# Performance work log

Hardware: AMD Instinct MI355X
Metric: run time of the kernel (lower is better)

## Reference

```python
import jax, jax.numpy as jnp
import numpy as np
from jax import lax

K = 16  # knn_k


def _mlp(x, W1, b1, W2, b2):
    h = jax.nn.gelu(x @ W1 + b1, approximate=False)  # torch nn.GELU default = exact
    return h @ W2 + b2


def setup_inputs() -> dict:
    key = jax.random.key(0)
    ks = jax.random.split(key, 10)
    B, N, F, H = 8, 4096, 64, 128

    def xav(k, shape):
        fan_in = shape[0]
        return (jax.random.normal(k, shape, jnp.float32) / np.sqrt(fan_in)).astype(jnp.float32)

    return {
        "coords": jax.random.normal(ks[0], (B, N, 3), jnp.float32),
        "features": jax.random.normal(ks[1], (B, N, F), jnp.float32),
        "inv_W1": xav(ks[2], (6, H)), "inv_b1": jnp.zeros((H,), jnp.float32),
        "inv_W2": xav(ks[3], (H, H)), "inv_b2": jnp.zeros((H,), jnp.float32),
        "feat_W1": xav(ks[4], (F, H)), "feat_b1": jnp.zeros((H,), jnp.float32),
        "feat_W2": xav(ks[5], (H, H)), "feat_b2": jnp.zeros((H,), jnp.float32),
        "sh_W1": xav(ks[6], (2 * H, H)), "sh_b1": jnp.zeros((H,), jnp.float32),
        "sh_W2": xav(ks[7], (H, H)), "sh_b2": jnp.zeros((H,), jnp.float32),
        "g0_W": xav(ks[8], (H, 1)), "g0_b": jnp.zeros((1,), jnp.float32),
    }


def _local_geometry(coords):
    # coords: [B,N,3]
    B, N, _ = coords.shape
    k = min(K, N - 1)
    # squared pairwise distances (monotone in euclidean dist -> same kNN indices)
    sq = jnp.sum(coords * coords, axis=-1)                    # [B,N]
    dist2 = sq[:, :, None] + sq[:, None, :] - 2.0 * jnp.einsum("bnd,bmd->bnm", coords, coords)
    dist2 = lax.stop_gradient(dist2)
    eye = jnp.eye(N, dtype=bool)
    dist2 = jnp.where(eye[None], jnp.inf, dist2)
    _, idx = lax.top_k(-dist2, k)                             # smallest-k -> [B,N,k]
    neighbors = jax.vmap(lambda c, i: c[i])(coords, idx)      # [B,N,k,3]
    relative = neighbors - coords[:, :, None, :]              # [B,N,k,3]
    cov = jnp.einsum("bnki,bnkj->bnij", relative, relative) / float(k)  # [B,N,3,3]
    evals, evecs = jnp.linalg.eigh(cov)                       # ascending
    normals = evecs[..., 0]                                   # smallest-eigval eigenvector, [B,N,3]
    center = coords.mean(axis=1, keepdims=True)
    outward = coords - center
    orient = jnp.sign(jnp.sum(normals * outward, axis=-1, keepdims=True))
    orient = jnp.where(orient == 0, 1.0, orient)
    normals = normals * orient
    normals = normals / jnp.maximum(jnp.linalg.norm(normals, axis=-1, keepdims=True), 1e-6)
    radius = jnp.linalg.norm(relative, axis=-1).mean(axis=-1, keepdims=True)   # [B,N,1]
    centered_radius = jnp.linalg.norm(outward, axis=-1, keepdims=True)
    eig_sum = jnp.maximum(evals.sum(axis=-1, keepdims=True), 1e-6)
    dominance = evals[..., 2:3] / eig_sum
    invariants = jnp.concatenate([evals, radius, centered_radius, dominance], axis=-1)  # [B,N,6]
    return normals, invariants


def reference(coords, features, inv_W1, inv_b1, inv_W2, inv_b2,
              feat_W1, feat_b1, feat_W2, feat_b2,
              sh_W1, sh_b1, sh_W2, sh_b2, g0_W, g0_b):
    normals, invariants = _local_geometry(coords)
    inv_h = _mlp(invariants, inv_W1, inv_b1, inv_W2, inv_b2)
    feat_h = _mlp(features, feat_W1, feat_b1, feat_W2, feat_b2)
    hidden = _mlp(jnp.concatenate([inv_h, feat_h], axis=-1), sh_W1, sh_b1, sh_W2, sh_b2)
    scalar = hidden @ g0_W + g0_b                                   # grade 0, [B,N,1]
    plane = jnp.stack([normals[..., 0], normals[..., 1], -normals[..., 2],
                       -jnp.sum(coords * normals, axis=-1)], axis=-1)  # grade 1, [B,N,4]
    biv = jnp.concatenate([normals, jnp.zeros_like(normals)], axis=-1)  # grade 2, [B,N,6]
    point = jnp.concatenate([coords, jnp.ones(coords.shape[:-1] + (1,), coords.dtype)], axis=-1)  # grade 3 OPNS point
    zero4 = jnp.zeros(coords.shape[:-1] + (1,), coords.dtype)            # grade 4
    return jnp.concatenate([scalar, plane, biv, point, zero4], axis=-1)  # [B,N,16]
```

## Files before the change

### kernel.cpp

```cpp
#include <hip/hip_runtime.h>
#include <hip/hip_bf16.h>

#define BB 8
#define NN 4096
#define FF 64
#define HH 128
#define KNN 16

typedef __attribute__((ext_vector_type(8))) short bf16x8;
typedef __attribute__((ext_vector_type(4))) short bf16x4;
typedef __attribute__((ext_vector_type(4))) float f32x4;

#define OFF_iW2 0
#define OFF_fW1 16384
#define OFF_fW2 24576
#define OFF_sW1 40960
#define OFF_sW2 73728
#define HI_SZ   90112

__device__ __forceinline__ float sq3(float x, float y, float z) {
    return fmaf(z, z, fmaf(y, y, __fmul_rn(x, x)));
}
__device__ __forceinline__ float dist2f(float px, float py, float pz, float psq, float4 cc) {
    float t = fmaf(pz, cc.z, fmaf(py, cc.y, __fmul_rn(px, cc.x)));
    return __fsub_rn(__fadd_rn(psq, cc.w), __fmul_rn(2.0f, t));
}

__device__ __forceinline__ short f2bf(float x) {
    unsigned u = __float_as_uint(x);
    u += 0x7fffu + ((u >> 16) & 1u);
    return (short)(u >> 16);
}
__device__ __forceinline__ float bf2f(short s) {
    return __uint_as_float(((unsigned)(unsigned short)s) << 16);
}

extern "C" __global__ __launch_bounds__(256)
void k_prep(const float* __restrict__ coords, float4* __restrict__ coords4, float* __restrict__ center,
            const float* __restrict__ iW2, const float* __restrict__ fW1,
            const float* __restrict__ fW2, const float* __restrict__ sW1,
            const float* __restrict__ sW2, short* __restrict__ wbf) {
    const int bx = blockIdx.x, tid = threadIdx.x;
    __shared__ float rx[256], ry[256], rz[256];
    if (bx < 8) {
        const int b = bx;
        float sx = 0.f, sy = 0.f, sz = 0.f;
        for (int n = tid; n < NN; n += 256) {
            const float* c = coords + (size_t)(b * NN + n) * 3;
            float x = c[0], y = c[1], z = c[2];
            coords4[b * NN + n] = make_float4(x, y, z, sq3(x, y, z));
            sx += x; sy += y; sz += z;
        }
        rx[tid] = sx; ry[tid] = sy; rz[tid] = sz;
        __syncthreads();
        for (int s = 128; s > 0; s >>= 1) {
            if (tid < s) { rx[tid] += rx[tid + s]; ry[tid] += ry[tid + s]; rz[tid] += rz[tid + s]; }
            __syncthreads();
        }
        if (tid == 0) {
            center[b * 4 + 0] = rx[0] * (1.0f / NN);
            center[b * 4 + 1] = ry[0] * (1.0f / NN);
            center[b * 4 + 2] = rz[0] * (1.0f / NN);
        }
    } else {
        const int wb = bx - 8;
        const int w = wb >> 4;
        const int xb = wb & 15;
        const float* W; int K; int off;
        if (w == 0)      { W = iW2; K = 128; off = OFF_iW2; }
        else if (w == 1) { W = fW1; K = 64;  off = OFF_fW1; }
        else if (w == 2) { W = fW2; K = 128; off = OFF_fW2; }
        else if (w == 3) { W = sW1; K = 256; off = OFF_sW1; }
        else             { W = sW2; K = 128; off = OFF_sW2; }
        short* hi = wbf + off;
        short* lo = wbf + HI_SZ + off;
        const int total = K * 128;
        for (int e = xb * 256 + tid; e < total; e += 4096) {
            int j = e & 7, lane = (e >> 3) & 63, ct = (e >> 9) & 7, kb = e >> 12;
            int k = kb * 32 + (lane >> 4) * 8 + j;
            int n = ct * 16 + (lane & 15);
            float v = W[k * 128 + n];
            short h = f2bf(v);
            float r = v - bf2f(h);
            hi[e] = h; lo[e] = f2bf(r);
        }
    }
}

#define JROT(app, aqq, apq, arp, arq, vp0, vp1, vp2, vq0, vq1, vq2) { \
    float tau_ = (aqq - app) / (2.0f * apq); \
    float tt_ = copysignf(1.0f, tau_) / (fabsf(tau_) + sqrtf(1.0f + tau_ * tau_)); \
    if (apq == 0.0f) tt_ = 0.0f; \
    float cc_ = 1.0f / sqrtf(1.0f + tt_ * tt_); \
    float ss_ = tt_ * cc_; \
    float app_n = cc_*cc_*app - 2.0f*cc_*ss_*apq + ss_*ss_*aqq; \
    float aqq_n = ss_*ss_*app + 2.0f*cc_*ss_*apq + cc_*cc_*aqq; \
    float apq_n = cc_*ss_*(app - aqq) + (cc_*cc_ - ss_*ss_)*apq; \
    float arp_n = cc_*arp - ss_*arq; \
    float arq_n = ss_*arp + cc_*arq; \
    app = app_n; aqq = aqq_n; apq = apq_n; arp = arp_n; arq = arq_n; \
    float t0_ = cc_*vp0 - ss_*vq0, t1_ = cc_*vp1 - ss_*vq1, t2_ = cc_*vp2 - ss_*vq2; \
    vq0 = ss_*vp0 + cc_*vq0; vq1 = ss_*vp1 + cc_*vq1; vq2 = ss_*vp2 + cc_*vq2; \
    vp0 = t0_; vp1 = t1_; vp2 = t2_; }

#define SWAPF(a, b) { float sw_ = a; a = b; b = sw_; }

__device__ __forceinline__ void ce(float& a, float& b) {
    float mn = fminf(a, b);
    b = fmaxf(a, b);
    a = mn;
}

__device__ __forceinline__ void sort16(float (&d)[16]) {
    ce(d[0],d[1]); ce(d[2],d[3]); ce(d[0],d[2]); ce(d[1],d[3]); ce(d[1],d[2]);
    ce(d[4],d[5]); ce(d[6],d[7]); ce(d[4],d[6]); ce(d[5],d[7]); ce(d[5],d[6]);
    ce(d[0],d[4]); ce(d[2],d[6]); ce(d[2],d[4]);
    ce(d[1],d[5]); ce(d[3],d[7]); ce(d[3],d[5]);
    ce(d[1],d[2]); ce(d[3],d[4]); ce(d[5],d[6]);
    ce(d[8],d[9]); ce(d[10],d[11]); ce(d[8],d[10]); ce(d[9],d[11]); ce(d[9],d[10]);
    ce(d[12],d[13]); ce(d[14],d[15]); ce(d[12],d[14]); ce(d[13],d[15]); ce(d[13],d[14]);
    ce(d[8],d[12]); ce(d[10],d[14]); ce(d[10],d[12]);
    ce(d[9],d[13]); ce(d[11],d[15]); ce(d[11],d[13]);
    ce(d[9],d[10]); ce(d[11],d[12]); ce(d[13],d[14]);
    ce(d[0],d[8]); ce(d[4],d[12]); ce(d[4],d[8]);
    ce(d[2],d[10]); ce(d[6],d[14]); ce(d[6],d[10]);
    ce(d[2],d[4]); ce(d[6],d[8]); ce(d[10],d[12]);
    ce(d[1],d[9]); ce(d[5],d[13]); ce(d[5],d[9]);
    ce(d[3],d[11]); ce(d[7],d[15]); ce(d[7],d[11]);
    ce(d[3],d[5]); ce(d[7],d[9]); ce(d[11],d[13]);
    ce(d[1],d[2]); ce(d[3],d[4]); ce(d[5],d[6]); ce(d[7],d[8]);
    ce(d[9],d[10]); ce(d[11],d[12]); ce(d[13],d[14]);
}

__device__ __forceinline__ void merge16(float (&dk)[16], float (&d)[16]) {
#pragma unroll
    for (int i = 0; i < 8; i++) {
        float a  = fminf(dk[i], d[15 - i]);
        float b2 = fminf(dk[15 - i], d[i]);
        d[i] = a; d[15 - i] = b2;
    }
#pragma unroll
    for (int j = 8; j > 0; j >>= 1)
#pragma unroll
        for (int i = 0; i < 16; i++) {
            int l = i ^ j;
            if (l > i) ce(d[i], d[l]);
        }
#pragma unroll
    for (int i = 0; i < 16; i++) dk[i] = d[i];
}

__device__ __forceinline__ void sort16i(int (&d)[16]) {
#pragma unroll
    for (int k = 2; k <= 16; k <<= 1) {
#pragma unroll
        for (int j = k >> 1; j > 0; j >>= 1) {
#pragma unroll
            for (int i = 0; i < 16; i++) {
                int l = i ^ j;
                if (l > i) {
                    int a = d[i], bq = d[l];
                    int mn = a < bq ? a : bq;
                    int mx = a < bq ? bq : a;
                    if ((i & k) == 0) { d[i] = mn; d[l] = mx; }
                    else              { d[i] = mx; d[l] = mn; }
                }
            }
        }
    }
}

__device__ __forceinline__ float gelu_exact(float x) {
    return 0.5f * x * (1.0f + erff(x * 0.70710678118654752440f));
}

template <int KB, bool INIT>
__device__ __forceinline__ void gemm_mfma(const short* Ab, const short* __restrict__ whi,
                                          const short* __restrict__ wlo,
                                          const float* __restrict__ bias,
                                          int wid, int lane, f32x4 acc[2]) {
    const int m16 = lane & 15, quad = lane >> 4;
    if (INIT) {
        float b0 = bias[wid * 16 + m16];
        acc[0] = (f32x4){b0, b0, b0, b0};
        acc[1] = acc[0];
    }
#pragma unroll 1
    for (int kb = 0; kb < KB; kb++) {
        bf16x8 a0 = *(const bf16x8*)(Ab + m16 * 136 + kb * 32 + quad * 8);
        bf16x8 a1 = *(const bf16x8*)(Ab + (m16 + 16) * 136 + kb * 32 + quad * 8);
        const int off = ((kb * 8 + wid) * 64 + lane) * 8;
        bf16x8 bh = *(const bf16x8*)(whi + off);
        bf16x8 bl = *(const bf16x8*)(wlo + off);
        acc[0] = __builtin_amdgcn_mfma_f32_16x16x32_bf16(a0, bh, acc[0], 0, 0, 0);
        acc[0] = __builtin_amdgcn_mfma_f32_16x16x32_bf16(a0, bl, acc[0], 0, 0, 0);
        acc[1] = __builtin_amdgcn_mfma_f32_16x16x32_bf16(a1, bh, acc[1], 0, 0, 0);
        acc[1] = __builtin_amdgcn_mfma_f32_16x16x32_bf16(a1, bl, acc[1], 0, 0, 0);
    }
}

__device__ __forceinline__ void acc_to_bf(short* dst, f32x4 acc[2], int wid, int lane, bool dogelu) {
    const int m16 = lane & 15, quad = lane >> 4;
#pragma unroll
    for (int mt = 0; mt < 2; mt++)
#pragma unroll
        for (int i = 0; i < 4; i++) {
            float v = acc[mt][i];
            if (dogelu) v = gelu_exact(v);
            dst[(mt * 16 + quad * 4 + i) * 136 + wid * 16 + m16] = f2bf(v);
        }
}

extern "C" __global__ __launch_bounds__(512, 8)
void k_fused(const float4* __restrict__ coords4, const float* __restrict__ center,
             const float* __restrict__ features, const short* __restrict__ wbf,
             const float* __restrict__ iW1, const float* __restrict__ ib1,
             const float* __restrict__ ib2,
             const float* __restrict__ fb1, const float* __restrict__ fb2,
             const float* __restrict__ sb1, const float* __restrict__ sb2,
             const float* __restrict__ gW, const float* __restrict__ gb,
             float* __restrict__ out) {
    const int blk = blockIdx.x;
    const int b = blk >> 7;
    const int chunk = blk & 127;
    const int tid = threadIdx.x;
    const int h = tid & 15;
    const int pid = tid >> 4;
    const int n = chunk * 32 + pid;
    const float4* __restrict__ C = coords4 + b * NN;

    __shared__ __align__(16) char smem[20352];
    unsigned short* slist = (unsigned short*)(smem);
    unsigned short* tlist = (unsigned short*)(smem + 1024);
    int* cnt_s = (int*)(smem + 1536);
    int* cnt_t = (int*)(smem + 1664);
    float* inv8 = (float*)(smem + 1792);
    float* sc   = (float*)(smem + 2816);
    short* Abf  = (short*)(smem + 2944);
    short* FHbf = (short*)(smem + 11648);

    if (tid < 32) { cnt_s[tid] = 0; cnt_t[tid] = 0; }

    float4 me = C[n];
    const float px = me.x, py = me.y, pz = me.z, psq = me.w;
    const float INF = __builtin_inff();
    const int self_j = ((n & 15) == h) ? (n >> 4) : 256;

    float dk[KNN];
#pragma unroll
    for (int i = 0; i < KNN; i++) dk[i] = INF;

    for (int bt = 0; bt < 16; bt++) {
        float d[16];
#pragma unroll
        for (int i = 0; i < 16; i++) {
            float4 cc = C[(bt * 16 + i) * 16 + h];
            float dd = dist2f(px, py, pz, psq, cc);
            d[i] = (bt * 16 + i) == self_j ? INF : dd;
        }
        sort16(d);
        merge16(dk, d);
    }

#pragma unroll
    for (int m = 1; m <= 8; m <<= 1) {
        float o[16];
#pragma unroll
        for (int i = 0; i < KNN; i++) o[i] = __shfl_xor(dk[i], m);
        merge16(dk, o);
    }
    const float d15 = dk[15];

    __syncthreads();

#pragma unroll 4
    for (int j = 0; j < 256; j++) {
        float4 cc = C[j * 16 + h];
        float d = dist2f(px, py, pz, psq, cc);
        if (j != self_j && d <= d15) {
            if (d < d15) {
                int pos = atomicAdd(&cnt_s[pid], 1);
                if (pos < 16) slist[pid * 16 + pos] = (unsigned short)(j * 16 + h);
            } else {
                int pos = atomicAdd(&cnt_t[pid], 1);
                if (pos < 8) tlist[pid * 8 + pos] = (unsigned short)(j * 16 + h);
            }
        }
    }
    __syncthreads();

    if (tid < 32) {
        const int np = chunk * 32 + tid;
        float4 pme = C[np];
        int ns = cnt_s[tid]; ns = ns > 15 ? 15 : ns;
        int ids[16];
#pragma unroll
        for (int j = 0; j < 16; j++) {
            int tj = j - ns; tj = tj < 0 ? 0 : (tj > 7 ? 7 : tj);
            int sid = (int)slist[tid * 16 + j];
            int tie = (int)tlist[tid * 8 + tj];
            ids[j] = (j < ns) ? sid : tie;
        }
        sort16i(ids);

        float cxx = 0.f, cxy = 0.f, cxz = 0.f, cyy = 0.f, cyz = 0.f, czz = 0.f, radsum = 0.f;
#pragma unroll
        for (int j = 0; j < KNN; j++) {
            float4 cc = C[ids[j]];
            float rx = __fsub_rn(cc.x, pme.x), ry = __fsub_rn(cc.y, pme.y), rz = __fsub_rn(cc.z, pme.z);
            cxx = __fadd_rn(cxx, __fmul_rn(rx, rx));
            cxy = __fadd_rn(cxy, __fmul_rn(rx, ry));
            cxz = __fadd_rn(cxz, __fmul_rn(rx, rz));
            cyy = __fadd_rn(cyy, __fmul_rn(ry, ry));
            cyz = __fadd_rn(cyz, __fmul_rn(ry, rz));
            czz = __fadd_rn(czz, __fmul_rn(rz, rz));
            float rr = __fadd_rn(__fadd_rn(__fmul_rn(rx, rx), __fmul_rn(ry, ry)), __fmul_rn(rz, rz));
            radsum = __fadd_rn(radsum, sqrtf(rr));
        }
        const float inv_k = 1.0f / KNN;
        float a00 = cxx * inv_k, a01 = cxy * inv_k, a02 = cxz * inv_k;
        float a11 = cyy * inv_k, a12 = cyz * inv_k, a22 = czz * inv_k;

        float V00 = 1.f, V01 = 0.f, V02 = 0.f;
        float V10 = 0.f, V11 = 1.f, V12 = 0.f;
        float V20 = 0.f, V21 = 0.f, V22 = 1.f;
        for (int sweep = 0; sweep < 6; sweep++) {
            JROT(a00, a11, a01, a02, a12, V00, V10, V20, V01, V11, V21);
            JROT(a00, a22, a02, a01, a12, V00, V10, V20, V02, V12, V22);
            JROT(a11, a22, a12, a01, a02, V01, V11, V21, V02, V12, V22);
        }
        float e0 = a00, e1 = a11, e2 = a22;
        float x0 = V00, y0 = V10, z0 = V20;
        float x1 = V01, y1 = V11, z1 = V21;
        float x2 = V02, y2 = V12, z2 = V22;
        if (e0 > e1) { SWAPF(e0, e1); SWAPF(x0, x1); SWAPF(y0, y1); SWAPF(z0, z1); }
        if (e1 > e2) { SWAPF(e1, e2); SWAPF(x1, x2); SWAPF(y1, y2); SWAPF(z1, z2); }
        if (e0 > e1) { SWAPF(e0, e1); SWAPF(x0, x1); SWAPF(y0, y1); SWAPF(z0, z1); }

        float cx = center[b * 4 + 0], cy = center[b * 4 + 1], cz = center[b * 4 + 2];
        float ox = __fsub_rn(pme.x, cx), oy = __fsub_rn(pme.y, cy), oz = __fsub_rn(pme.z, cz);
        float dt = __fadd_rn(__fadd_rn(__fmul_rn(x0, ox), __fmul_rn(y0, oy)), __fmul_rn(z0, oz));
        float sgn = (dt >= 0.0f) ? 1.0f : -1.0f;
        x0 *= sgn; y0 *= sgn; z0 *= sgn;
        float nrm = sqrtf(__fadd_rn(__fadd_rn(__fmul_rn(x0, x0), __fmul_rn(y0, y0)), __fmul_rn(z0, z0)));
        float den = fmaxf(nrm, 1e-6f);
        x0 = x0 / den; y0 = y0 / den; z0 = z0 / den;

        float radius = radsum * inv_k;
        float crad = sqrtf(__fadd_rn(__fadd_rn(__fmul_rn(ox, ox), __fmul_rn(oy, oy)), __fmul_rn(oz, oz)));
        float esum = fmaxf(__fadd_rn(__fadd_rn(e0, e1), e2), 1e-6f);
        float dom = e2 / esum;

        float* ip = inv8 + tid * 8;
        ip[0] = e0; ip[1] = e1; ip[2] = e2; ip[3] = radius; ip[4] = crad; ip[5] = dom;
        ip[6] = 0.f; ip[7] = 0.f;

        float pd = __fadd_rn(__fadd_rn(__fmul_rn(pme.x, x0), __fmul_rn(pme.y, y0)), __fmul_rn(pme.z, z0));
        float4* o = (float4*)(out + (size_t)(b * NN + np) * 16);
        o[0] = make_float4(0.0f, x0, y0, -z0);
        o[1] = make_float4(-pd, x0, y0, z0);
        o[2] = make_float4(0.0f, 0.0f, 0.0f, pme.x);
        o[3] = make_float4(pme.y, pme.z, 1.0f, 0.0f);
        sc[tid] = gb[0];
    }
    __syncthreads();

    const int wid = tid >> 6, lane = tid & 63;
    const short* w_iW2h = wbf + OFF_iW2; const short* w_iW2l = wbf + HI_SZ + OFF_iW2;
    const short* w_fW1h = wbf + OFF_fW1; const short* w_fW1l = wbf + HI_SZ + OFF_fW1;
    const short* w_fW2h = wbf + OFF_fW2; const short* w_fW2l = wbf + HI_SZ + OFF_fW2;
    const short* w_sW1h = wbf + OFF_sW1; const short* w_sW1l = wbf + HI_SZ + OFF_sW1;
    const short* w_sW2h = wbf + OFF_sW2; const short* w_sW2l = wbf + HI_SZ + OFF_sW2;
    f32x4 acc[2];

    {
        int row = tid >> 4, c4 = (tid & 15) * 4;
        const float* s = features + (size_t)(b * NN + chunk * 32 + row) * FF + c4;
        float4 v = *(const float4*)s;
        bf16x4 pk;
        pk[0] = f2bf(v.x); pk[1] = f2bf(v.y); pk[2] = f2bf(v.z); pk[3] = f2bf(v.w);
        *(bf16x4*)(Abf + row * 136 + c4) = pk;
    }
    __syncthreads();

    gemm_mfma<2, true>(Abf, w_fW1h, w_fW1l, fb1, wid, lane, acc);
    __syncthreads();
    acc_to_bf(Abf, acc, wid, lane, true);
    __syncthreads();

    gemm_mfma<4, true>(Abf, w_fW2h, w_fW2l, fb2, wid, lane, acc);
    __syncthreads();
    acc_to_bf(FHbf, acc, wid, lane, false);

    {
        const int cg = tid & 31, pg = tid >> 5;
        const int c0 = cg * 4, p0 = pg * 2;
        float4 bb = *(const float4*)(ib1 + c0);
        float a2[2][4];
#pragma unroll
        for (int i = 0; i < 2; i++) { a2[i][0] = bb.x; a2[i][1] = bb.y; a2[i][2] = bb.z; a2[i][3] = bb.w; }
#pragma unroll
        for (int k = 0; k < 6; k++) {
            float4 w = *(const float4*)(iW1 + k * HH + c0);
#pragma unroll
            for (int i = 0; i < 2; i++) {
                float a = inv8[(p0 + i) * 8 + k];
                a2[i][0] = fmaf(a, w.x, a2[i][0]);
                a2[i][1] = fmaf(a, w.y, a2[i][1]);
                a2[i][2] = fmaf(a, w.z, a2[i][2]);
                a2[i][3] = fmaf(a, w.w, a2[i][3]);
            }
        }
#pragma unroll
        for (int i = 0; i < 2; i++) {
            bf16x4 pk;
            pk[0] = f2bf(gelu_exact(a2[i][0])); pk[1] = f2bf(gelu_exact(a2[i][1]));
            pk[2] = f2bf(gelu_exact(a2[i][2])); pk[3] = f2bf(gelu_exact(a2[i][3]));
            *(bf16x4*)(Abf + (p0 + i) * 136 + c0) = pk;
        }
    }
    __syncthreads();

    gemm_mfma<4, true>(Abf, w_iW2h, w_iW2l, ib2, wid, lane, acc);
    __syncthreads();
    acc_to_bf(Abf, acc, wid, lane, false);
    __syncthreads();

    gemm_mfma<4, true>(Abf, w_sW1h, w_sW1l, sb1, wid, lane, acc);
    gemm_mfma<4, false>(FHbf, w_sW1h + 16384, w_sW1l + 16384, nullptr, wid, lane, acc);
    __syncthreads();
    acc_to_bf(Abf, acc, wid, lane, true);
    __syncthreads();

    gemm_mfma<4, true>(Abf, w_sW2h, w_sW2l, sb2, wid, lane, acc);
    {
        const int m16 = lane & 15, quad = lane >> 4;
        float g = gW[wid * 16 + m16];
#pragma unroll
        for (int mt = 0; mt < 2; mt++)
#pragma unroll
            for (int i = 0; i < 4; i++)
                atomicAdd(&sc[mt * 16 + quad * 4 + i], acc[mt][i] * g);
    }
    __syncthreads();
    if (tid < 32) out[(size_t)(b * NN + chunk * 32 + tid) * 16] = sc[tid];
}

extern "C" void kernel_launch(void* const* d_in, const int* in_sizes, int n_in,
                              void* d_out, int out_size, void* d_ws, size_t ws_size,
                              hipStream_t stream) {
    const float* coords   = (const float*)d_in[0];
    const float* features = (const float*)d_in[1];
    const float* iW1 = (const float*)d_in[2],  * ib1 = (const float*)d_in[3];
    const float* iW2 = (const float*)d_in[4],  * ib2 = (const float*)d_in[5];
    const float* fW1 = (const float*)d_in[6],  * fb1 = (const float*)d_in[7];
    const float* fW2 = (const float*)d_in[8],  * fb2 = (const float*)d_in[9];
    const float* sW1 = (const float*)d_in[10], * sb1 = (const float*)d_in[11];
    const float* sW2 = (const float*)d_in[12], * sb2 = (const float*)d_in[13];
    const float* gW  = (const float*)d_in[14], * gb  = (const float*)d_in[15];
    float* out = (float*)d_out;

    float* ws = (float*)d_ws;
    float4* coords4 = (float4*)ws;
    float* center = ws + BB * NN * 4;
    short* wbf = (short*)((char*)d_ws + 524416);

    hipLaunchKernelGGL(k_prep, dim3(88), dim3(256), 0, stream,
                       coords, coords4, center, iW2, fW1, fW2, sW1, sW2, wbf);
    hipLaunchKernelGGL(k_fused, dim3(1024), dim3(512), 0, stream, coords4, center, features, wbf,
                       iW1, ib1, ib2, fb1, fb2, sb1, sb2, gW, gb, out);
}
```

Measured before the change: 295.9 us.

## Split fused kernel into kNN and MLP kernels, stage coords in LDS tiles

The fused kernel is split into a kNN/geometry kernel and an MLP kernel. The invariants are passed between them through a global workspace buffer. The kNN kernel now stages 1024-point coordinate tiles in shared memory and reads the candidates from LDS instead of from global memory in both the distance pass and the collection pass. Each kernel also gets its own smaller shared-memory footprint. The cost is an extra kernel launch, an extra global round trip for the invariants, and extra block barriers per tile.

```diff
diff --git a/kernel.cpp b/kernel.cpp
--- a/kernel.cpp
+++ b/kernel.cpp
@@ -170,6 +170,161 @@
     }
 }
 
+extern "C" __global__ __launch_bounds__(512, 8)
+void k_knn(const float4* __restrict__ coords4, const float* __restrict__ center,
+           float* __restrict__ inv8g, float* __restrict__ out) {
+    const int blk = blockIdx.x;
+    const int b = blk >> 7;
+    const int chunk = blk & 127;
+    const int tid = threadIdx.x;
+    const int h = tid & 15;
+    const int pid = tid >> 4;
+    const int n = chunk * 32 + pid;
+    const float4* __restrict__ C = coords4 + b * NN;
+
+    __shared__ __align__(16) float4 tile[1024];
+    __shared__ unsigned short slist[512];
+    __shared__ unsigned short tlist[256];
+    __shared__ int cnt_s[32];
+    __shared__ int cnt_t[32];
+
+    if (tid < 32) { cnt_s[tid] = 0; cnt_t[tid] = 0; }
+
+    float4 me = C[n];
+    const float px = me.x, py = me.y, pz = me.z, psq = me.w;
+    const float INF = __builtin_inff();
+
+    float dk[KNN];
+#pragma unroll
+    for (int i = 0; i < KNN; i++) dk[i] = INF;
+
+    for (int r = 0; r < 4; r++) {
+        __syncthreads();
+        tile[tid] = C[r * 1024 + tid];
+        tile[tid + 512] = C[r * 1024 + tid + 512];
+        __syncthreads();
+#pragma unroll
+        for (int bt = 0; bt < 4; bt++) {
+            float d[16];
+#pragma unroll
+            for (int i = 0; i < 16; i++) {
+                float4 cc = tile[bt * 256 + i * 16 + h];
+                float dd = dist2f(px, py, pz, psq, cc);
+                int g = r * 1024 + bt * 256 + i * 16 + h;
+                d[i] = (g == n) ? INF : dd;
+            }
+            sort16(d);
+            merge16(dk, d);
+        }
+    }
+
+#pragma unroll
+    for (int m = 1; m <= 8; m <<= 1) {
+        float o[16];
+#pragma unroll
+        for (int i = 0; i < KNN; i++) o[i] = __shfl_xor(dk[i], m);
+        merge16(dk, o);
+    }
+    const float d15 = dk[15];
+
+    for (int r = 0; r < 4; r++) {
+        __syncthreads();
+        tile[tid] = C[r * 1024 + tid];
+        tile[tid + 512] = C[r * 1024 + tid + 512];
+        __syncthreads();
+#pragma unroll 4
+        for (int j16 = 0; j16 < 64; j16++) {
+            float4 cc = tile[j16 * 16 + h];
+            float d = dist2f(px, py, pz, psq, cc);
+            int g = r * 1024 + j16 * 16 + h;
+            if (g != n && d <= d15) {
+                if (d < d15) {
+                    int pos = atomicAdd(&cnt_s[pid], 1);
+                    if (pos < 16) slist[pid * 16 + pos] = (unsigned short)g;
+                } else {
+                    int pos = atomicAdd(&cnt_t[pid], 1);
+                    if (pos < 8) tlist[pid * 8 + pos] = (unsigned short)g;
+                }
+            }
+        }
+    }
+    __syncthreads();
+
+    if (tid < 32) {
+        const int np = chunk * 32 + tid;
+        float4 pme = C[np];
+        int ns = cnt_s[tid]; ns = ns > 15 ? 15 : ns;
+        int ids[16];
+#pragma unroll
+        for (int j = 0; j < 16; j++) {
+            int tj = j - ns; tj = tj < 0 ? 0 : (tj > 7 ? 7 : tj);
+            int sid = (int)slist[tid * 16 + j];
+            int tie = (int)tlist[tid * 8 + tj];
+            ids[j] = (j < ns) ? sid : tie;
+        }
+        sort16i(ids);
+
+        float cxx = 0.f, cxy = 0.f, cxz = 0.f, cyy = 0.f, cyz = 0.f, czz = 0.f, radsum = 0.f;
+#pragma unroll
+        for (int j = 0; j < KNN; j++) {
+            float4 cc = C[ids[j]];
+            float rx = __fsub_rn(cc.x, pme.x), ry = __fsub_rn(cc.y, pme.y), rz = __fsub_rn(cc.z, pme.z);
+            cxx = __fadd_rn(cxx, __fmul_rn(rx, rx));
+            cxy = __fadd_rn(cxy, __fmul_rn(rx, ry));
+            cxz = __fadd_rn(cxz, __fmul_rn(rx, rz));
+            cyy = __fadd_rn(cyy, __fmul_rn(ry, ry));
+            cyz = __fadd_rn(cyz, __fmul_rn(ry, rz));
+            czz = __fadd_rn(czz, __fmul_rn(rz, rz));
+            float rr = __fadd_rn(__fadd_rn(__fmul_rn(rx, rx), __fmul_rn(ry, ry)), __fmul_rn(rz, rz));
+            radsum = __fadd_rn(radsum, sqrtf(rr));
+        }
+        const float inv_k = 1.0f / KNN;
+        float a00 = cxx * inv_k, a01 = cxy * inv_k, a02 = cxz * inv_k;
+        float a11 = cyy * inv_k, a12 = cyz * inv_k, a22 = czz * inv_k;
+
+        float V00 = 1.f, V01 = 0.f, V02 = 0.f;
+        float V10 = 0.f, V11 = 1.f, V12 = 0.f;
+        float V20 = 0.f, V21 = 0.f, V22 = 1.f;
+        for (int sweep = 0; sweep < 6; sweep++) {
+            JROT(a00, a11, a01, a02, a12, V00, V10, V20, V01, V11, V21);
+            JROT(a00, a22, a02, a01, a12, V00, V10, V20, V02, V12, V22);
+            JROT(a11, a22, a12, a01, a02, V01, V11, V21, V02, V12, V22);
+        }
+        float e0 = a00, e1 = a11, e2 = a22;
+        float x0 = V00, y0 = V10, z0 = V20;
+        float x1 = V01, y1 = V11, z1 = V21;
+        float x2 = V02, y2 = V12, z2 = V22;
+        if (e0 > e1) { SWAPF(e0, e1); SWAPF(x0, x1); SWAPF(y0, y1); SWAPF(z0, z1); }
+        if (e1 > e2) { SWAPF(e1, e2); SWAPF(x1, x2); SWAPF(y1, y2); SWAPF(z1, z2); }
+        if (e0 > e1) { SWAPF(e0, e1); SWAPF(x0, x1); SWAPF(y0, y1); SWAPF(z0, z1); }
+
+        float cx = center[b * 4 + 0], cy = center[b * 4 + 1], cz = center[b * 4 + 2];
+        float ox = __fsub_rn(pme.x, cx), oy = __fsub_rn(pme.y, cy), oz = __fsub_rn(pme.z, cz);
+        float dt = __fadd_rn(__fadd_rn(__fmul_rn(x0, ox), __fmul_rn(y0, oy)), __fmul_rn(z0, oz));
+        float sgn = (dt >= 0.0f) ? 1.0f : -1.0f;
+        x0 *= sgn; y0 *= sgn; z0 *= sgn;
+        float nrm = sqrtf(__fadd_rn(__fadd_rn(__fmul_rn(x0, x0), __fmul_rn(y0, y0)), __fmul_rn(z0, z0)));
+        float den = fmaxf(nrm, 1e-6f);
+        x0 = x0 / den; y0 = y0 / den; z0 = z0 / den;
+
+        float radius = radsum * inv_k;
+        float crad = sqrtf(__fadd_rn(__fadd_rn(__fmul_rn(ox, ox), __fmul_rn(oy, oy)), __fmul_rn(oz, oz)));
+        float esum = fmaxf(__fadd_rn(__fadd_rn(e0, e1), e2), 1e-6f);
+        float dom = e2 / esum;
+
+        float* ip = inv8g + (size_t)(b * NN + np) * 8;
+        ip[0] = e0; ip[1] = e1; ip[2] = e2; ip[3] = radius; ip[4] = crad; ip[5] = dom;
+        ip[6] = 0.f; ip[7] = 0.f;
+
+        float pd = __fadd_rn(__fadd_rn(__fmul_rn(pme.x, x0), __fmul_rn(pme.y, y0)), __fmul_rn(pme.z, z0));
+        float4* o = (float4*)(out + (size_t)(b * NN + np) * 16);
+        o[0] = make_float4(0.0f, x0, y0, -z0);
+        o[1] = make_float4(-pd, x0, y0, z0);
+        o[2] = make_float4(0.0f, 0.0f, 0.0f, pme.x);
+        o[3] = make_float4(pme.y, pme.z, 1.0f, 0.0f);
+    }
+}
+
 __device__ __forceinline__ float gelu_exact(float x) {
     return 0.5f * x * (1.0f + erff(x * 0.70710678118654752440f));
 }
@@ -212,158 +367,22 @@
 }
 
 extern "C" __global__ __launch_bounds__(512, 8)
-void k_fused(const float4* __restrict__ coords4, const float* __restrict__ center,
-             const float* __restrict__ features, const short* __restrict__ wbf,
-             const float* __restrict__ iW1, const float* __restrict__ ib1,
-             const float* __restrict__ ib2,
-             const float* __restrict__ fb1, const float* __restrict__ fb2,
-             const float* __restrict__ sb1, const float* __restrict__ sb2,
-             const float* __restrict__ gW, const float* __restrict__ gb,
-             float* __restrict__ out) {
+void k_mlp(const float* __restrict__ features, const short* __restrict__ wbf,
+           const float* __restrict__ iW1, const float* __restrict__ ib1,
+           const float* __restrict__ ib2,
+           const float* __restrict__ fb1, const float* __restrict__ fb2,
+           const float* __restrict__ sb1, const float* __restrict__ sb2,
+           const float* __restrict__ gW, const float* __restrict__ gb,
+           const float* __restrict__ inv8g, float* __restrict__ out) {
     const int blk = blockIdx.x;
     const int b = blk >> 7;
     const int chunk = blk & 127;
     const int tid = threadIdx.x;
-    const int h = tid & 15;
-    const int pid = tid >> 4;
-    const int n = chunk * 32 + pid;
-    const float4* __restrict__ C = coords4 + b * NN;
-
-    __shared__ __align__(16) char smem[20352];
-    unsigned short* slist = (unsigned short*)(smem);
-    unsigned short* tlist = (unsigned short*)(smem + 1024);
-    int* cnt_s = (int*)(smem + 1536);
-    int* cnt_t = (int*)(smem + 1664);
-    float* inv8 = (float*)(smem + 1792);
-    float* sc   = (float*)(smem + 2816);
-    short* Abf  = (short*)(smem + 2944);
-    short* FHbf = (short*)(smem + 11648);
-
-    if (tid < 32) { cnt_s[tid] = 0; cnt_t[tid] = 0; }
-
-    float4 me = C[n];
-    const float px = me.x, py = me.y, pz = me.z, psq = me.w;
-    const float INF = __builtin_inff();
-    const int self_j = ((n & 15) == h) ? (n >> 4) : 256;
-
-    float dk[KNN];
-#pragma unroll
-    for (int i = 0; i < KNN; i++) dk[i] = INF;
-
-    for (int bt = 0; bt < 16; bt++) {
-        float d[16];
-#pragma unroll
-        for (int i = 0; i < 16; i++) {
-            float4 cc = C[(bt * 16 + i) * 16 + h];
-            float dd = dist2f(px, py, pz, psq, cc);
-            d[i] = (bt * 16 + i) == self_j ? INF : dd;
-        }
-        sort16(d);
-        merge16(dk, d);
-    }
-
-#pragma unroll
-    for (int m = 1; m <= 8; m <<= 1) {
-        float o[16];
-#pragma unroll
-        for (int i = 0; i < KNN; i++) o[i] = __shfl_xor(dk[i], m);
-        merge16(dk, o);
-    }
-    const float d15 = dk[15];
-
-    __syncthreads();
-
-#pragma unroll 4
-    for (int j = 0; j < 256; j++) {
-        float4 cc = C[j * 16 + h];
-        float d = dist2f(px, py, pz, psq, cc);
-        if (j != self_j && d <= d15) {
-            if (d < d15) {
-                int pos = atomicAdd(&cnt_s[pid], 1);
-                if (pos < 16) slist[pid * 16 + pos] = (unsigned short)(j * 16 + h);
-            } else {
-                int pos = atomicAdd(&cnt_t[pid], 1);
-                if (pos < 8) tlist[pid * 8 + pos] = (unsigned short)(j * 16 + h);
-            }
-        }
-    }
-    __syncthreads();
-
-    if (tid < 32) {
-        const int np = chunk * 32 + tid;
-        float4 pme = C[np];
-        int ns = cnt_s[tid]; ns = ns > 15 ? 15 : ns;
-        int ids[16];
-#pragma unroll
-        for (int j = 0; j < 16; j++) {
-            int tj = j - ns; tj = tj < 0 ? 0 : (tj > 7 ? 7 : tj);
-            int sid = (int)slist[tid * 16 + j];
-            int tie = (int)tlist[tid * 8 + tj];
-            ids[j] = (j < ns) ? sid : tie;
-        }
-        sort16i(ids);
-
-        float cxx = 0.f, cxy = 0.f, cxz = 0.f, cyy = 0.f, cyz = 0.f, czz = 0.f, radsum = 0.f;
-#pragma unroll
-        for (int j = 0; j < KNN; j++) {
-            float4 cc = C[ids[j]];
-            float rx = __fsub_rn(cc.x, pme.x), ry = __fsub_rn(cc.y, pme.y), rz = __fsub_rn(cc.z, pme.z);
-            cxx = __fadd_rn(cxx, __fmul_rn(rx, rx));
-            cxy = __fadd_rn(cxy, __fmul_rn(rx, ry));
-            cxz = __fadd_rn(cxz, __fmul_rn(rx, rz));
-            cyy = __fadd_rn(cyy, __fmul_rn(ry, ry));
-            cyz = __fadd_rn(cyz, __fmul_rn(ry, rz));
-            czz = __fadd_rn(czz, __fmul_rn(rz, rz));
-            float rr = __fadd_rn(__fadd_rn(__fmul_rn(rx, rx), __fmul_rn(ry, ry)), __fmul_rn(rz, rz));
-            radsum = __fadd_rn(radsum, sqrtf(rr));
-        }
-        const float inv_k = 1.0f / KNN;
-        float a00 = cxx * inv_k, a01 = cxy * inv_k, a02 = cxz * inv_k;
-        float a11 = cyy * inv_k, a12 = cyz * inv_k, a22 = czz * inv_k;
-
-        float V00 = 1.f, V01 = 0.f, V02 = 0.f;
-        float V10 = 0.f, V11 = 1.f, V12 = 0.f;
-        float V20 = 0.f, V21 = 0.f, V22 = 1.f;
-        for (int sweep = 0; sweep < 6; sweep++) {
-            JROT(a00, a11, a01, a02, a12, V00, V10, V20, V01, V11, V21);
-            JROT(a00, a22, a02, a01, a12, V00, V10, V20, V02, V12, V22);
-            JROT(a11, a22, a12, a01, a02, V01, V11, V21, V02, V12, V22);
-        }
-        float e0 = a00, e1 = a11, e2 = a22;
-        float x0 = V00, y0 = V10, z0 = V20;
-        float x1 = V01, y1 = V11, z1 = V21;
-        float x2 = V02, y2 = V12, z2 = V22;
-        if (e0 > e1) { SWAPF(e0, e1); SWAPF(x0, x1); SWAPF(y0, y1); SWAPF(z0, z1); }
-        if (e1 > e2) { SWAPF(e1, e2); SWAPF(x1, x2); SWAPF(y1, y2); SWAPF(z1, z2); }
-        if (e0 > e1) { SWAPF(e0, e1); SWAPF(x0, x1); SWAPF(y0, y1); SWAPF(z0, z1); }
-
-        float cx = center[b * 4 + 0], cy = center[b * 4 + 1], cz = center[b * 4 + 2];
-        float ox = __fsub_rn(pme.x, cx), oy = __fsub_rn(pme.y, cy), oz = __fsub_rn(pme.z, cz);
-        float dt = __fadd_rn(__fadd_rn(__fmul_rn(x0, ox), __fmul_rn(y0, oy)), __fmul_rn(z0, oz));
-        float sgn = (dt >= 0.0f) ? 1.0f : -1.0f;
-        x0 *= sgn; y0 *= sgn; z0 *= sgn;
-        float nrm = sqrtf(__fadd_rn(__fadd_rn(__fmul_rn(x0, x0), __fmul_rn(y0, y0)), __fmul_rn(z0, z0)));
-        float den = fmaxf(nrm, 1e-6f);
-        x0 = x0 / den; y0 = y0 / den; z0 = z0 / den;
-
-        float radius = radsum * inv_k;
-        float crad = sqrtf(__fadd_rn(__fadd_rn(__fmul_rn(ox, ox), __fmul_rn(oy, oy)), __fmul_rn(oz, oz)));
-        float esum = fmaxf(__fadd_rn(__fadd_rn(e0, e1), e2), 1e-6f);
-        float dom = e2 / esum;
-
-        float* ip = inv8 + tid * 8;
-        ip[0] = e0; ip[1] = e1; ip[2] = e2; ip[3] = radius; ip[4] = crad; ip[5] = dom;
-        ip[6] = 0.f; ip[7] = 0.f;
-
-        float pd = __fadd_rn(__fadd_rn(__fmul_rn(pme.x, x0), __fmul_rn(pme.y, y0)), __fmul_rn(pme.z, z0));
-        float4* o = (float4*)(out + (size_t)(b * NN + np) * 16);
-        o[0] = make_float4(0.0f, x0, y0, -z0);
-        o[1] = make_float4(-pd, x0, y0, z0);
-        o[2] = make_float4(0.0f, 0.0f, 0.0f, pme.x);
-        o[3] = make_float4(pme.y, pme.z, 1.0f, 0.0f);
-        sc[tid] = gb[0];
-    }
-    __syncthreads();
+
+    __shared__ __align__(16) float inv8[256];
+    __shared__ float sc[32];
+    __shared__ __align__(16) short Abf[32 * 136];
+    __shared__ __align__(16) short FHbf[32 * 136];
 
     const int wid = tid >> 6, lane = tid & 63;
     const short* w_iW2h = wbf + OFF_iW2; const short* w_iW2l = wbf + HI_SZ + OFF_iW2;
@@ -373,6 +392,8 @@
     const short* w_sW2h = wbf + OFF_sW2; const short* w_sW2l = wbf + HI_SZ + OFF_sW2;
     f32x4 acc[2];
 
+    if (tid < 256) inv8[tid] = inv8g[(size_t)(b * NN + chunk * 32) * 8 + tid];
+    if (tid < 32) sc[tid] = gb[0];
     {
         int row = tid >> 4, c4 = (tid & 15) * 4;
         const float* s = features + (size_t)(b * NN + chunk * 32 + row) * FF + c4;
@@ -460,13 +481,15 @@
     const float* gW  = (const float*)d_in[14], * gb  = (const float*)d_in[15];
     float* out = (float*)d_out;
 
-    float* ws = (float*)d_ws;
+    char* ws = (char*)d_ws;
     float4* coords4 = (float4*)ws;
-    float* center = ws + BB * NN * 4;
-    short* wbf = (short*)((char*)d_ws + 524416);
+    float* center   = (float*)(ws + 524288);
+    short* wbf      = (short*)(ws + 524416);
+    float* inv8g    = (float*)(ws + 884864);
 
     hipLaunchKernelGGL(k_prep, dim3(88), dim3(256), 0, stream,
                        coords, coords4, center, iW2, fW1, fW2, sW1, sW2, wbf);
-    hipLaunchKernelGGL(k_fused, dim3(1024), dim3(512), 0, stream, coords4, center, features, wbf,
-                       iW1, ib1, ib2, fb1, fb2, sb1, sb2, gW, gb, out);
-}
+    hipLaunchKernelGGL(k_knn, dim3(1024), dim3(512), 0, stream, coords4, center, inv8g, out);
+    hipLaunchKernelGGL(k_mlp, dim3(1024), dim3(512), 0, stream, features, wbf,
+                       iW1, ib1, ib2, fb1, fb2, sb1, sb2, gW, gb, inv8g, out);
+}
```

Result: faster. 263.8 us (-10.9%).
